# Optimization experiments

Measured on AMD Instinct MI355X. Metric: run time of the kernel, lower is better.

Reference implementation:

```python
import jax, jax.numpy as jnp
import numpy as np

NUM_HEADS = 4
QK_DIM = 32
HEAD_DIM = QK_DIM // NUM_HEADS  # 8
SCALE = HEAD_DIM ** (-0.5)


def conv1x1(x, w, b):
    # x: [B, Cin, T, N], w: [Cout, Cin], b: [Cout]
    return jnp.einsum('bdtn,od->botn', x, w) + b[None, :, None, None]


def _to_heads(t):
    # t: [B, C, T, N] -> [B, T, H, N, C//H]
    B, C, T, N = t.shape
    return t.transpose(0, 2, 3, 1).reshape(B, T, N, NUM_HEADS, C // NUM_HEADS).transpose(0, 1, 3, 2, 4)


def _attn_block(x1, wq, bq, wk, bk, wv, bv, mask):
    q = _to_heads(conv1x1(x1, wq, bq))  # [B,T,H,N,hd]
    k = _to_heads(conv1x1(x1, wk, bk))
    v = _to_heads(conv1x1(x1, wv, bv))  # [B,T,H,N,vd]
    s = jnp.einsum('bthnd,bthmd->bthnm', q, k) * SCALE  # [B,T,H,N,N]
    if mask is not None:
        s = jnp.where(mask, -jnp.inf, s)
    a = jax.nn.softmax(s, axis=-1)
    o = jnp.einsum('bthnm,bthmd->bthnd', a, v)  # [B,T,H,N,vd]
    B, T, H, N, vd = o.shape
    # faithful to torch: (B,T,H,N,vd).transpose(1,2) -> (B,H,T,N,vd), then reshape(B,N,T,-1)
    return o.transpose(0, 2, 1, 3, 4).reshape(B, N, T, H * vd)


def setup_inputs() -> dict:
    key = jax.random.key(0)
    ks = jax.random.split(key, 16)
    B, D, T, N = 8, 64, 12, 512
    CIN, QK, COUT = 32, 32, 32
    inp = {}
    inp['x'] = jax.random.normal(ks[0], (B, D, T, N), dtype=jnp.float32)
    inp['geo_mask'] = jax.random.randint(ks[1], (N, N), 0, 2) > 0
    inp['w_proj1'] = jax.random.normal(ks[2], (CIN, D), dtype=jnp.float32) * 0.05
    inp['b_proj1'] = jax.random.normal(ks[3], (CIN,), dtype=jnp.float32) * 0.05
    inp['wgq'] = jax.random.normal(ks[4], (QK, CIN), dtype=jnp.float32) * 0.05
    inp['bgq'] = jax.random.normal(ks[5], (QK,), dtype=jnp.float32) * 0.05
    inp['wgk'] = jax.random.normal(ks[6], (QK, CIN), dtype=jnp.float32) * 0.05
    inp['bgk'] = jax.random.normal(ks[7], (QK,), dtype=jnp.float32) * 0.05
    inp['wgv'] = jax.random.normal(ks[8], (COUT, CIN), dtype=jnp.float32) * 0.05
    inp['bgv'] = jax.random.normal(ks[9], (COUT,), dtype=jnp.float32) * 0.05
    inp['wq'] = jax.random.normal(ks[10], (QK, CIN), dtype=jnp.float32) * 0.05
    inp['bq'] = jax.random.normal(ks[11], (QK,), dtype=jnp.float32) * 0.05
    inp['wk'] = jax.random.normal(ks[12], (QK, CIN), dtype=jnp.float32) * 0.05
    inp['bk'] = jax.random.normal(ks[13], (QK,), dtype=jnp.float32) * 0.05
    inp['wv'] = jax.random.normal(ks[14], (COUT, CIN), dtype=jnp.float32) * 0.05
    inp['bv'] = jax.random.normal(ks[15], (COUT,), dtype=jnp.float32) * 0.05
    return inp


def reference(x, geo_mask, w_proj1, b_proj1, wgq, bgq, wgk, bgk, wgv, bgv, wq, bq, wk, bk, wv, bv):
    # Align(64,64) is identity
    x_in = x
    x1 = conv1x1(x, w_proj1, b_proj1)  # [B,32,T,N]
    x_geo_v = _attn_block(x1, wgq, bgq, wgk, bgk, wgv, bgv, geo_mask)  # [B,N,T,32]
    x_v = _attn_block(x1, wq, bq, wk, bk, wv, bv, None)                # [B,N,T,32]
    out = jnp.concatenate([x_v, x_geo_v], axis=-1).transpose(0, 3, 2, 1)  # [B,64,T,N]
    return jax.nn.relu(out + x_in)
```

## Files before the change

### kernel.cpp

```cpp
#include <hip/hip_runtime.h>
#include <hip/hip_bf16.h>

typedef __attribute__((ext_vector_type(4))) short bf16x4;
typedef __attribute__((ext_vector_type(16))) float f32x16;

#define SCALE 0.35355339059327373f
#define LOG2E 1.4426950408889634f

struct ProjW { const float* w[6]; const float* b[6]; };

template<typename T, typename F>
__device__ inline T bcast(F f) { union { F a; T b; } u; u.a = f; return u.b; }

__device__ inline unsigned pk2(float a, float b) {
  __hip_bfloat162 h = __float22bfloat162_rn(make_float2(a, b));
  return *(unsigned*)&h;
}

__device__ inline float fast_exp2(float x) {
  float r;
  asm("v_exp_f32 %0, %1" : "=v"(r) : "v"(x));
  return r;
}

__global__ void k_pack_mask(const int* __restrict__ mask, unsigned* __restrict__ mbw) {
  int w = blockIdx.x * 256 + threadIdx.x;
  int n = w >> 4, wi = w & 15;
  const int* mp = mask + n * 512 + wi * 32;
  unsigned bits = 0u;
  #pragma unroll
  for (int j = 0; j < 32; ++j) bits |= (mp[j] != 0) ? (1u << j) : 0u;
  mbw[w] = bits;
}

__global__ void k_wfuse(ProjW pw, const float* __restrict__ w1, const float* __restrict__ b1,
                        float* __restrict__ wfT, float* __restrict__ bfv) {
  int p = blockIdx.x;
  int d = threadIdx.x;
  const float* W = pw.w[p];
  float sc = (p % 3 == 0) ? SCALE * LOG2E : 1.0f;
  float col[32];
  #pragma unroll
  for (int e = 0; e < 32; ++e) col[e] = w1[e * 64 + d];
  for (int c = 0; c < 32; ++c) {
    float a = 0.f;
    #pragma unroll
    for (int e = 0; e < 32; ++e) a = fmaf(W[c * 32 + e], col[e], a);
    wfT[(p * 64 + d) * 32 + c] = a * sc;
  }
  if (d < 32) {
    float a = pw.b[p][d];
    #pragma unroll
    for (int e = 0; e < 32; ++e) a = fmaf(W[d * 32 + e], b1[e], a);
    bfv[p * 32 + d] = a * sc;
  }
}

__global__ void __launch_bounds__(384) k_qkv(const float* __restrict__ x,
    const float* __restrict__ wfT, const float* __restrict__ bfv,
    ushort* __restrict__ Qb, ushort* __restrict__ Kb, ushort* __restrict__ Vt) {
  __shared__ float Wl[12288];
  __shared__ unsigned xs32[4096];
  int bt = blockIdx.x;
  int ch = blockIdx.y;
  int tid = threadIdx.x;
  int n0 = ch * 128;
  int b = bt / 12, t = bt - b * 12;
  const float* xb = x + ((size_t)b * 768 + t) * 512 + n0;
  for (int i = tid; i < 4096; i += 384) {
    int d = i >> 6, np = i & 63;
    float2 v = *(const float2*)(xb + (size_t)d * 6144 + 2 * np);
    xs32[d * 64 + np] = pk2(v.x, v.y);
  }
  for (int i = tid; i < 12288; i += 384) Wl[i] = wfT[i];
  __syncthreads();

  int p = tid >> 6;
  int nl = tid & 63;
  const float* W = Wl + p * 2048;
  float accA[32], accB[32];
  #pragma unroll
  for (int c = 0; c < 32; ++c) { accA[c] = bfv[p * 32 + c]; accB[c] = accA[c]; }
  #pragma unroll 8
  for (int d = 0; d < 64; ++d) {
    unsigned xu = xs32[d * 64 + nl];
    float xa = __uint_as_float(xu << 16);
    float xbv = __uint_as_float(xu & 0xffff0000u);
    #pragma unroll
    for (int c4 = 0; c4 < 8; ++c4) {
      float4 w = *(const float4*)(W + d * 32 + c4 * 4);
      accA[c4*4+0] = fmaf(w.x, xa, accA[c4*4+0]); accB[c4*4+0] = fmaf(w.x, xbv, accB[c4*4+0]);
      accA[c4*4+1] = fmaf(w.y, xa, accA[c4*4+1]); accB[c4*4+1] = fmaf(w.y, xbv, accB[c4*4+1]);
      accA[c4*4+2] = fmaf(w.z, xa, accA[c4*4+2]); accB[c4*4+2] = fmaf(w.z, xbv, accB[c4*4+2]);
      accA[c4*4+3] = fmaf(w.w, xa, accA[c4*4+3]); accB[c4*4+3] = fmaf(w.w, xbv, accB[c4*4+3]);
    }
  }

  int blk = p / 3, m = p - blk * 3;
  int n = n0 + 2 * nl;
  if (m < 2) {
    ushort* dst = (m == 0) ? Qb : Kb;
    #pragma unroll
    for (int h = 0; h < 4; ++h) {
      size_t inst = ((size_t)blk * 96 + bt) * 4 + h;
      uint4 uA, uB;
      uA.x = pk2(accA[h*8+0], accA[h*8+1]); uA.y = pk2(accA[h*8+2], accA[h*8+3]);
      uA.z = pk2(accA[h*8+4], accA[h*8+5]); uA.w = pk2(accA[h*8+6], accA[h*8+7]);
      uB.x = pk2(accB[h*8+0], accB[h*8+1]); uB.y = pk2(accB[h*8+2], accB[h*8+3]);
      uB.z = pk2(accB[h*8+4], accB[h*8+5]); uB.w = pk2(accB[h*8+6], accB[h*8+7]);
      *(uint4*)(dst + (inst * 512 + n) * 8)     = uA;
      *(uint4*)(dst + (inst * 512 + n + 1) * 8) = uB;
    }
  } else {
    #pragma unroll
    for (int h = 0; h < 4; ++h) {
      size_t inst = ((size_t)blk * 96 + bt) * 4 + h;
      #pragma unroll
      for (int dd = 0; dd < 8; ++dd)
        *(unsigned*)(Vt + (inst * 8 + dd) * 512 + n) = pk2(accA[h*8+dd], accB[h*8+dd]);
    }
  }
}

__global__ void __launch_bounds__(512) k_attn(const ushort* __restrict__ Qb,
    const ushort* __restrict__ Kb, const ushort* __restrict__ Vt,
    const unsigned* __restrict__ mbw, float* __restrict__ obuf) {
  __shared__ __align__(16) ushort Kl[512 * 12];
  __shared__ __align__(16) ushort Vl[9 * 520];
  int h = blockIdx.x, bt = blockIdx.y, blk = blockIdx.z;
  int tid = threadIdx.x;
  size_t inst = ((size_t)blk * 96 + bt) * 4 + h;

  {
    uint4 kr = ((const uint4*)(Kb + inst * 4096))[tid];
    *(uint2*)&Kl[tid * 12]     = make_uint2(kr.x, kr.y);
    *(uint2*)&Kl[tid * 12 + 4] = make_uint2(kr.z, kr.w);
  }
  {
    const ushort* vp = Vt + inst * 4096;
    #pragma unroll
    for (int d = 0; d < 8; ++d) Vl[d * 520 + tid] = vp[d * 512 + tid];
    Vl[8 * 520 + tid] = 0x3F80;
  }
  __syncthreads();

  int lane = tid & 63, lo = lane & 31, hi = lane >> 5, w = tid >> 6;
  int qbase = w * 64;

  bf16x4 qf[2];
  #pragma unroll
  for (int s = 0; s < 2; ++s) {
    int q = qbase + s * 32 + lo;
    qf[s] = bcast<bf16x4>(*(const uint2*)(Qb + inst * 4096 + q * 8 + hi * 4));
  }

  f32x16 acc[2], zc;
  #pragma unroll
  for (int i = 0; i < 16; ++i) { acc[0][i] = 0.f; acc[1][i] = 0.f; zc[i] = 0.f; }

  for (int t16 = 0; t16 < 16; ++t16) {
    bf16x4 kf = bcast<bf16x4>(*(const uint2*)&Kl[(t16 * 32 + lo) * 12 + 4 * hi]);
    bf16x4 vf[4];
    int vrow = (lo < 8 ? lo : 8) * 520 + t16 * 32 + 4 * hi;
    #pragma unroll
    for (int c = 0; c < 4; ++c) {
      uint2 vv = *(const uint2*)&Vl[vrow + 8 * c];
      if (lo > 8) { vv.x = 0u; vv.y = 0u; }
      vf[c] = bcast<bf16x4>(vv);
    }
    #pragma unroll
    for (int s = 0; s < 2; ++s) {
      f32x16 st = __builtin_amdgcn_mfma_f32_32x32x8bf16_1k(kf, qf[s], zc, 0, 0, 0);
      unsigned mwh = 0u;
      if (blk == 1) {
        int q = qbase + s * 32 + lo;
        mwh = mbw[q * 16 + t16] >> (4 * hi);
      }
      unsigned u[8];
      #pragma unroll
      for (int j = 0; j < 8; ++j) {
        float p0 = fast_exp2(st[2*j]);
        float p1 = fast_exp2(st[2*j+1]);
        if (blk == 1) {
          int c0 = ((2*j) & 3) + 8 * ((2*j) >> 2);
          if ((mwh >> c0) & 1u) p0 = 0.f;
          if ((mwh >> (c0 + 1)) & 1u) p1 = 0.f;
        }
        u[j] = (__float_as_uint(p0) >> 16) | (__float_as_uint(p1) & 0xffff0000u);
      }
      #pragma unroll
      for (int c = 0; c < 4; ++c) {
        uint2 pu = make_uint2(u[2 * c], u[2 * c + 1]);
        acc[s] = __builtin_amdgcn_mfma_f32_32x32x8bf16_1k(vf[c], bcast<bf16x4>(pu), acc[s], 0, 0, 0);
      }
    }
  }

  int b = bt / 12, t = bt - b * 12;
  #pragma unroll
  for (int s = 0; s < 2; ++s) {
    float l = __shfl(acc[s][4], lo);
    float inv = __builtin_amdgcn_rcpf(l);
    int q = qbase + s * 32 + lo;
    int g = (h * 12 + t) * 128 + (q >> 2);
    float* ob = obuf + (size_t)blk * 1572864 + ((size_t)b * 6144 + g) * 32 + (q & 3) * 8 + 4 * hi;
    *(float4*)ob = make_float4(acc[s][0] * inv, acc[s][1] * inv, acc[s][2] * inv, acc[s][3] * inv);
  }
}

__global__ void __launch_bounds__(256) k_out(const float* __restrict__ x, const float* __restrict__ obuf,
                     float* __restrict__ out) {
  __shared__ float tile[64][65];
  int nc = blockIdx.x;
  int tq = blockIdx.y;
  int b  = blockIdx.z;
  int n0 = nc * 64;
  #pragma unroll
  for (int it = 0; it < 16; ++it) {
    int i = it * 256 + threadIdx.x;
    int nl = i >> 6, c = i & 63;
    int sel = c >> 5;
    tile[nl][c] = obuf[(size_t)sel * 1572864 +
                       ((size_t)b * 6144 + (size_t)(n0 + nl) * 12 + tq) * 32 + (c & 31)];
  }
  __syncthreads();
  #pragma unroll
  for (int it = 0; it < 16; ++it) {
    int i = it * 256 + threadIdx.x;
    int c = i >> 6, nl = i & 63;
    size_t oi = ((size_t)(b * 64 + c) * 12 + tq) * 512 + n0 + nl;
    out[oi] = fmaxf(tile[nl][c] + x[oi], 0.f);
  }
}

extern "C" void kernel_launch(void* const* d_in, const int* in_sizes, int n_in,
                              void* d_out, int out_size, void* d_ws, size_t ws_size,
                              hipStream_t stream) {
  const float* x        = (const float*)d_in[0];
  const int*   geo_mask = (const int*)d_in[1];
  const float* w_proj1  = (const float*)d_in[2];
  const float* b_proj1  = (const float*)d_in[3];
  ProjW pw;
  pw.w[0] = (const float*)d_in[10]; pw.b[0] = (const float*)d_in[11];
  pw.w[1] = (const float*)d_in[12]; pw.b[1] = (const float*)d_in[13];
  pw.w[2] = (const float*)d_in[14]; pw.b[2] = (const float*)d_in[15];
  pw.w[3] = (const float*)d_in[4];  pw.b[3] = (const float*)d_in[5];
  pw.w[4] = (const float*)d_in[6];  pw.b[4] = (const float*)d_in[7];
  pw.w[5] = (const float*)d_in[8];  pw.b[5] = (const float*)d_in[9];
  float* out = (float*)d_out;

  float* ws = (float*)d_ws;
  float* obuf = ws;
  float* wfT  = ws + 3145728;
  float* bfv  = ws + 3158016;
  unsigned* mbw = (unsigned*)(ws + 3158208);
  ushort* Qb = (ushort*)(ws + 3166400);
  ushort* Kb = (ushort*)(ws + 4739264);
  ushort* Vt = (ushort*)(ws + 6312128);

  k_pack_mask<<<32, 256, 0, stream>>>(geo_mask, mbw);
  k_wfuse<<<6, 64, 0, stream>>>(pw, w_proj1, b_proj1, wfT, bfv);
  k_qkv<<<dim3(96, 4), 384, 0, stream>>>(x, wfT, bfv, Qb, Kb, Vt);
  k_attn<<<dim3(4, 96, 2), 512, 0, stream>>>(Qb, Kb, Vt, mbw, obuf);
  k_out<<<dim3(8, 12, 8), 256, 0, stream>>>(x, obuf, out);
}
```

Baseline: 189.9 us.

## Compute fused QKV projection with bf16 MFMA instead of scalar FMAs

The QKV projection kernel now keeps the fused weights in bf16 (padded rows of 68) and does the 64-deep contraction with 32x32x8 bf16 MFMA tiles rather than per-thread scalar FMA loops. It also drops the LDS staging of x and reads it straight from global memory into MFMA fragments. The grid is doubled so each block covers 64 tokens. Rounding to bf16 now truncates instead of round-to-nearest, which adds a small precision loss. The Vt writes are now scattered 16-bit stores.

Measured after the change: 162.8 us. 14.3% less time.

```diff
diff --git a/kernel.cpp b/kernel.cpp
--- a/kernel.cpp
+++ b/kernel.cpp
@@ -12,9 +12,8 @@
 template<typename T, typename F>
 __device__ inline T bcast(F f) { union { F a; T b; } u; u.a = f; return u.b; }
 
-__device__ inline unsigned pk2(float a, float b) {
-  __hip_bfloat162 h = __float22bfloat162_rn(make_float2(a, b));
-  return *(unsigned*)&h;
+__device__ inline unsigned tpk2(float a, float b) {
+  return (__float_as_uint(a) >> 16) | (__float_as_uint(b) & 0xffff0000u);
 }
 
 __device__ inline float fast_exp2(float x) {
@@ -34,7 +33,7 @@
 }
 
 __global__ void k_wfuse(ProjW pw, const float* __restrict__ w1, const float* __restrict__ b1,
-                        float* __restrict__ wfT, float* __restrict__ bfv) {
+                        ushort* __restrict__ wfb, float* __restrict__ bfv) {
   int p = blockIdx.x;
   int d = threadIdx.x;
   const float* W = pw.w[p];
@@ -46,7 +45,8 @@
     float a = 0.f;
     #pragma unroll
     for (int e = 0; e < 32; ++e) a = fmaf(W[c * 32 + e], col[e], a);
-    wfT[(p * 64 + d) * 32 + c] = a * sc;
+    __hip_bfloat16 hb = __float2bfloat16(a * sc);
+    wfb[(p * 32 + c) * 68 + d] = *(ushort*)&hb;
   }
   if (d < 32) {
     float a = pw.b[p][d];
@@ -57,67 +57,77 @@
 }
 
 __global__ void __launch_bounds__(384) k_qkv(const float* __restrict__ x,
-    const float* __restrict__ wfT, const float* __restrict__ bfv,
+    const ushort* __restrict__ wfb, const float* __restrict__ bfv,
     ushort* __restrict__ Qb, ushort* __restrict__ Kb, ushort* __restrict__ Vt) {
-  __shared__ float Wl[12288];
-  __shared__ unsigned xs32[4096];
-  int bt = blockIdx.x;
-  int ch = blockIdx.y;
+  __shared__ __align__(16) ushort Wl[192 * 68];
+  int bt = blockIdx.x, ch = blockIdx.y;
   int tid = threadIdx.x;
-  int n0 = ch * 128;
   int b = bt / 12, t = bt - b * 12;
-  const float* xb = x + ((size_t)b * 768 + t) * 512 + n0;
-  for (int i = tid; i < 4096; i += 384) {
-    int d = i >> 6, np = i & 63;
-    float2 v = *(const float2*)(xb + (size_t)d * 6144 + 2 * np);
-    xs32[d * 64 + np] = pk2(v.x, v.y);
-  }
-  for (int i = tid; i < 12288; i += 384) Wl[i] = wfT[i];
+  for (int i = tid; i < 6528; i += 384)
+    ((unsigned*)Wl)[i] = ((const unsigned*)wfb)[i];
   __syncthreads();
 
-  int p = tid >> 6;
-  int nl = tid & 63;
-  const float* W = Wl + p * 2048;
-  float accA[32], accB[32];
-  #pragma unroll
-  for (int c = 0; c < 32; ++c) { accA[c] = bfv[p * 32 + c]; accB[c] = accA[c]; }
-  #pragma unroll 8
-  for (int d = 0; d < 64; ++d) {
-    unsigned xu = xs32[d * 64 + nl];
-    float xa = __uint_as_float(xu << 16);
-    float xbv = __uint_as_float(xu & 0xffff0000u);
-    #pragma unroll
-    for (int c4 = 0; c4 < 8; ++c4) {
-      float4 w = *(const float4*)(W + d * 32 + c4 * 4);
-      accA[c4*4+0] = fmaf(w.x, xa, accA[c4*4+0]); accB[c4*4+0] = fmaf(w.x, xbv, accB[c4*4+0]);
-      accA[c4*4+1] = fmaf(w.y, xa, accA[c4*4+1]); accB[c4*4+1] = fmaf(w.y, xbv, accB[c4*4+1]);
-      accA[c4*4+2] = fmaf(w.z, xa, accA[c4*4+2]); accB[c4*4+2] = fmaf(w.z, xbv, accB[c4*4+2]);
-      accA[c4*4+3] = fmaf(w.w, xa, accA[c4*4+3]); accB[c4*4+3] = fmaf(w.w, xbv, accB[c4*4+3]);
-    }
-  }
-
-  int blk = p / 3, m = p - blk * 3;
-  int n = n0 + 2 * nl;
-  if (m < 2) {
-    ushort* dst = (m == 0) ? Qb : Kb;
-    #pragma unroll
-    for (int h = 0; h < 4; ++h) {
-      size_t inst = ((size_t)blk * 96 + bt) * 4 + h;
-      uint4 uA, uB;
-      uA.x = pk2(accA[h*8+0], accA[h*8+1]); uA.y = pk2(accA[h*8+2], accA[h*8+3]);
-      uA.z = pk2(accA[h*8+4], accA[h*8+5]); uA.w = pk2(accA[h*8+6], accA[h*8+7]);
-      uB.x = pk2(accB[h*8+0], accB[h*8+1]); uB.y = pk2(accB[h*8+2], accB[h*8+3]);
-      uB.z = pk2(accB[h*8+4], accB[h*8+5]); uB.w = pk2(accB[h*8+6], accB[h*8+7]);
-      *(uint4*)(dst + (inst * 512 + n) * 8)     = uA;
-      *(uint4*)(dst + (inst * 512 + n + 1) * 8) = uB;
-    }
-  } else {
-    #pragma unroll
-    for (int h = 0; h < 4; ++h) {
-      size_t inst = ((size_t)blk * 96 + bt) * 4 + h;
-      #pragma unroll
-      for (int dd = 0; dd < 8; ++dd)
-        *(unsigned*)(Vt + (inst * 8 + dd) * 512 + n) = pk2(accA[h*8+dd], accB[h*8+dd]);
+  int lane = tid & 63, ci = tid >> 6;
+  int lo = lane & 31, hi = lane >> 5;
+  int blk = ci / 3, m = ci - blk * 3;
+
+  bf16x4 af[8];
+  #pragma unroll
+  for (int ks = 0; ks < 8; ++ks)
+    af[ks] = *(const bf16x4*)&Wl[(32 * ci + lo) * 68 + 8 * ks + 4 * hi];
+
+  float bias[16];
+  #pragma unroll
+  for (int r = 0; r < 16; ++r)
+    bias[r] = bfv[ci * 32 + (r & 3) + 8 * (r >> 2) + 4 * hi];
+
+  const float* xb = x + ((size_t)b * 768 + t) * 512;
+  for (int tile = 0; tile < 2; ++tile) {
+    int n = ch * 64 + tile * 32 + lo;
+    uint2 bfr[8];
+    #pragma unroll
+    for (int ks = 0; ks < 8; ++ks) {
+      int d0 = 8 * ks + 4 * hi;
+      float x0 = xb[(size_t)(d0 + 0) * 6144 + n];
+      float x1 = xb[(size_t)(d0 + 1) * 6144 + n];
+      float x2 = xb[(size_t)(d0 + 2) * 6144 + n];
+      float x3 = xb[(size_t)(d0 + 3) * 6144 + n];
+      bfr[ks] = make_uint2(tpk2(x0, x1), tpk2(x2, x3));
+    }
+    f32x16 acc;
+    #pragma unroll
+    for (int i = 0; i < 16; ++i) acc[i] = 0.f;
+    #pragma unroll
+    for (int ks = 0; ks < 8; ++ks)
+      acc = __builtin_amdgcn_mfma_f32_32x32x8bf16_1k(af[ks], bcast<bf16x4>(bfr[ks]), acc, 0, 0, 0);
+    #pragma unroll
+    for (int r = 0; r < 16; ++r) acc[r] += bias[r];
+
+    if (m < 2) {
+      ushort* dst = (m == 0) ? Qb : Kb;
+      #pragma unroll
+      for (int h = 0; h < 4; ++h) {
+        size_t inst = ((size_t)blk * 96 + bt) * 4 + h;
+        unsigned u0 = tpk2(acc[4*h + 0], acc[4*h + 1]);
+        unsigned u1 = tpk2(acc[4*h + 2], acc[4*h + 3]);
+        unsigned u0x = __shfl_xor(u0, 32);
+        unsigned u1x = __shfl_xor(u1, 32);
+        if (hi == 0) {
+          uint4 u = make_uint4(u0, u1, u0x, u1x);
+          *(uint4*)(dst + (inst * 512 + n) * 8) = u;
+        }
+      }
+    } else {
+      #pragma unroll
+      for (int j = 0; j < 8; ++j) {
+        int r = 2 * j;
+        int h = r >> 2;
+        int dd = (r & 3) + 4 * hi;
+        size_t inst = ((size_t)blk * 96 + bt) * 4 + h;
+        unsigned u = tpk2(acc[r], acc[r + 1]);
+        Vt[(inst * 8 + dd) * 512 + n]     = (ushort)(u & 0xffffu);
+        Vt[(inst * 8 + dd + 1) * 512 + n] = (ushort)(u >> 16);
+      }
     }
   }
 }
@@ -186,7 +196,7 @@
           if ((mwh >> c0) & 1u) p0 = 0.f;
           if ((mwh >> (c0 + 1)) & 1u) p1 = 0.f;
         }
-        u[j] = (__float_as_uint(p0) >> 16) | (__float_as_uint(p1) & 0xffff0000u);
+        u[j] = tpk2(p0, p1);
       }
       #pragma unroll
       for (int c = 0; c < 4; ++c) {
@@ -251,16 +261,16 @@
 
   float* ws = (float*)d_ws;
   float* obuf = ws;
-  float* wfT  = ws + 3145728;
-  float* bfv  = ws + 3158016;
-  unsigned* mbw = (unsigned*)(ws + 3158208);
-  ushort* Qb = (ushort*)(ws + 3166400);
-  ushort* Kb = (ushort*)(ws + 4739264);
-  ushort* Vt = (ushort*)(ws + 6312128);
+  float* bfv  = ws + 3145728;
+  ushort* wfb = (ushort*)(ws + 3145920);
+  unsigned* mbw = (unsigned*)(ws + 3152448);
+  ushort* Qb = (ushort*)(ws + 3160640);
+  ushort* Kb = (ushort*)(ws + 4733504);
+  ushort* Vt = (ushort*)(ws + 6306368);
 
   k_pack_mask<<<32, 256, 0, stream>>>(geo_mask, mbw);
-  k_wfuse<<<6, 64, 0, stream>>>(pw, w_proj1, b_proj1, wfT, bfv);
-  k_qkv<<<dim3(96, 4), 384, 0, stream>>>(x, wfT, bfv, Qb, Kb, Vt);
+  k_wfuse<<<6, 64, 0, stream>>>(pw, w_proj1, b_proj1, wfb, bfv);
+  k_qkv<<<dim3(96, 8), 384, 0, stream>>>(x, wfb, bfv, Qb, Kb, Vt);
   k_attn<<<dim3(4, 96, 2), 512, 0, stream>>>(Qb, Kb, Vt, mbw, obuf);
   k_out<<<dim3(8, 12, 8), 256, 0, stream>>>(x, obuf, out);
 }
```
